# Kernel optimization log

Measured on AMD Instinct MI355X. Metric: run time of the kernel, lower is better.

## Reference

```python
import jax, jax.numpy as jnp
import numpy as np


def _shift(x, n):
    # torch.roll along the last (angular) axis
    return jnp.roll(x, n, axis=3)


def _flip(x, n):
    # mirror about index n along the last axis: out[..., i] = x[..., (n - i) mod W]
    return jnp.roll(jnp.flip(x, axis=3), n + 1, axis=3)


def setup_inputs() -> dict:
    key = jax.random.key(0)
    k1, k2, k3 = jax.random.split(key, 3)
    B, C, H, W = 16, 96, 96, 96
    x = jax.random.normal(k1, (B, C, H, W), dtype=jnp.float32)
    s = jax.random.normal(k2, (B, 5), dtype=jnp.float32)
    w = jax.random.uniform(k3, (B, C, H, W), dtype=jnp.float32) + 0.1  # keep denominator well-conditioned
    return {"x": x, "s": s, "w": w}


def reference(x, s, w):
    # s.shape[1] == 5 branch of SymmetryControl (square symmetry: 3 rotations + 2 mirrors)
    sg = jax.nn.sigmoid(s).reshape(s.shape[0], -1, 1, 1)  # [B,5,1,1]
    step = x.shape[3] // 8

    x90 = _shift(x, step * 2)
    x180 = _shift(x, step * 4)
    x270 = _shift(x, step * 6)
    x90f = _flip(x, step * 2 - 1)
    x180f = _flip(x, step * 4 - 1)

    w90 = sg[:, 0:1] * _shift(w, step * 2)
    w180 = sg[:, 1:2] * _shift(w, step * 4)
    w270 = sg[:, 2:3] * _shift(w, step * 6)
    w90f = sg[:, 3:4] * _flip(w, step * 2 - 1)
    w180f = sg[:, 4:5] * _flip(w, step * 4 - 1)

    a = (w * x + w90 * x90 + w180 * x180 + w270 * x270
         + w90f * x90f + w180f * x180f)
    b = w + w90 + w180 + w270 + w90f + w180f
    return a / b
```

## Files before the change

### kernel.cpp

```cpp
#include <hip/hip_runtime.h>


#define WDIM  96
#define RPB   9216
#define WPB   4
#define PAIRS 8
#define RPW   (2 * PAIRS)

typedef float fvec3 __attribute__((ext_vector_type(3)));

__device__ __forceinline__ float bperm(int byteidx, float v) {
    return __int_as_float(__builtin_amdgcn_ds_bpermute(byteidx, __float_as_int(v)));
}

__global__ __launch_bounds__(64 * WPB)
void symctl_kernel(const float* __restrict__ x,
                   const float* __restrict__ s,
                   const float* __restrict__ w,
                   float* __restrict__ out) {
    const int lane = threadIdx.x & 63;
    const int tl   = lane & 31;
    const int hsel = lane & 32;
    const int h    = lane >> 5;

    const int wid  = blockIdx.x * WPB + (threadIdx.x >> 6);
    const int base = (RPW * wid + h) * WDIM + 3 * tl;

    fvec3 xa[PAIRS], wa[PAIRS];
#pragma unroll
    for (int k = 0; k < PAIRS; ++k)
        xa[k] = *(const fvec3*)(x + base + k * (2 * WDIM));
#pragma unroll
    for (int k = 0; k < PAIRS; ++k)
        wa[k] = *(const fvec3*)(w + base + k * (2 * WDIM));

    __builtin_amdgcn_sched_barrier(0);

    const int b = (blockIdx.x * (RPW * WPB)) / RPB;
    const float* sb = s + b * 5;
    const float sg0 = 1.0f / (1.0f + __expf(-sb[0]));
    const float sg1 = 1.0f / (1.0f + __expf(-sb[1]));
    const float sg2 = 1.0f / (1.0f + __expf(-sb[2]));
    const float sg3 = 1.0f / (1.0f + __expf(-sb[3]));
    const float sg4 = 1.0f / (1.0f + __expf(-sb[4]));

    const int i90  = (hsel | ((tl -  8) & 31)) << 2;
    const int i180 = (hsel | ((tl - 16) & 31)) << 2;
    const int i270 = (hsel | ((tl +  8) & 31)) << 2;
    const int f90  = (hsel | (( 7 - tl) & 31)) << 2;
    const int f180 = (hsel | ((15 - tl) & 31)) << 2;

#pragma unroll
    for (int k = 0; k < PAIRS; ++k) {
        const fvec3 xc = xa[k];
        const fvec3 wc = wa[k];

        const float p0 = xc.x * wc.x;
        const float p1 = xc.y * wc.y;
        const float p2 = xc.z * wc.z;

        float n0 = p0,   n1 = p1,   n2 = p2;
        float d0 = wc.x, d1 = wc.y, d2 = wc.z;

        n0 = fmaf(sg0, bperm(i90,  p0),   n0);
        n1 = fmaf(sg0, bperm(i90,  p1),   n1);
        n2 = fmaf(sg0, bperm(i90,  p2),   n2);
        d0 = fmaf(sg0, bperm(i90,  wc.x), d0);
        d1 = fmaf(sg0, bperm(i90,  wc.y), d1);
        d2 = fmaf(sg0, bperm(i90,  wc.z), d2);

        n0 = fmaf(sg1, bperm(i180, p0),   n0);
        n1 = fmaf(sg1, bperm(i180, p1),   n1);
        n2 = fmaf(sg1, bperm(i180, p2),   n2);
        d0 = fmaf(sg1, bperm(i180, wc.x), d0);
        d1 = fmaf(sg1, bperm(i180, wc.y), d1);
        d2 = fmaf(sg1, bperm(i180, wc.z), d2);

        n0 = fmaf(sg2, bperm(i270, p0),   n0);
        n1 = fmaf(sg2, bperm(i270, p1),   n1);
        n2 = fmaf(sg2, bperm(i270, p2),   n2);
        d0 = fmaf(sg2, bperm(i270, wc.x), d0);
        d1 = fmaf(sg2, bperm(i270, wc.y), d1);
        d2 = fmaf(sg2, bperm(i270, wc.z), d2);

        n0 = fmaf(sg3, bperm(f90,  p2),   n0);
        n1 = fmaf(sg3, bperm(f90,  p1),   n1);
        n2 = fmaf(sg3, bperm(f90,  p0),   n2);
        d0 = fmaf(sg3, bperm(f90,  wc.z), d0);
        d1 = fmaf(sg3, bperm(f90,  wc.y), d1);
        d2 = fmaf(sg3, bperm(f90,  wc.x), d2);

        n0 = fmaf(sg4, bperm(f180, p2),   n0);
        n1 = fmaf(sg4, bperm(f180, p1),   n1);
        n2 = fmaf(sg4, bperm(f180, p0),   n2);
        d0 = fmaf(sg4, bperm(f180, wc.z), d0);
        d1 = fmaf(sg4, bperm(f180, wc.y), d1);
        d2 = fmaf(sg4, bperm(f180, wc.x), d2);

        fvec3 o;
        o.x = n0 * __builtin_amdgcn_rcpf(d0);
        o.y = n1 * __builtin_amdgcn_rcpf(d1);
        o.z = n2 * __builtin_amdgcn_rcpf(d2);
        __builtin_nontemporal_store(o, (fvec3*)(out + base + k * (2 * WDIM)));
    }
}

extern "C" void kernel_launch(void* const* d_in, const int* in_sizes, int n_in,
                              void* d_out, int out_size, void* d_ws, size_t ws_size,
                              hipStream_t stream) {
    const float* x = (const float*)d_in[0];
    const float* s = (const float*)d_in[1];
    const float* w = (const float*)d_in[2];
    float* out = (float*)d_out;

    const int n_rows = in_sizes[0] / WDIM;
    const int waves  = n_rows / RPW;
    const int grid   = waves / WPB;

    dim3 block(64 * WPB);
    symctl_kernel<<<grid, block, 0, stream>>>(x, s, w, out);
}
```

Baseline: 154.6 us.

## Use inline-asm split loads with staged vmcnt waits and halve rows per wave

```diff
diff --git a/kernel.cpp b/kernel.cpp
--- a/kernel.cpp
+++ b/kernel.cpp
@@ -4,10 +4,10 @@
 #define WDIM  96
 #define RPB   9216
 #define WPB   4
-#define PAIRS 8
+#define PAIRS 4
 #define RPW   (2 * PAIRS)
 
-typedef float fvec3 __attribute__((ext_vector_type(3)));
+typedef float v2f __attribute__((ext_vector_type(2)));
 
 __device__ __forceinline__ float bperm(int byteidx, float v) {
     return __int_as_float(__builtin_amdgcn_ds_bpermute(byteidx, __float_as_int(v)));
@@ -24,17 +24,7 @@
     const int h    = lane >> 5;
 
     const int wid  = blockIdx.x * WPB + (threadIdx.x >> 6);
-    const int base = (RPW * wid + h) * WDIM + 3 * tl;
-
-    fvec3 xa[PAIRS], wa[PAIRS];
-#pragma unroll
-    for (int k = 0; k < PAIRS; ++k)
-        xa[k] = *(const fvec3*)(x + base + k * (2 * WDIM));
-#pragma unroll
-    for (int k = 0; k < PAIRS; ++k)
-        wa[k] = *(const fvec3*)(w + base + k * (2 * WDIM));
-
-    __builtin_amdgcn_sched_barrier(0);
+    const int voff = ((RPW * wid + h) * WDIM + 3 * tl) * 4;
 
     const int b = (blockIdx.x * (RPW * WPB)) / RPB;
     const float* sb = s + b * 5;
@@ -50,59 +40,91 @@
     const int f90  = (hsel | (( 7 - tl) & 31)) << 2;
     const int f180 = (hsel | ((15 - tl) & 31)) << 2;
 
-#pragma unroll
-    for (int k = 0; k < PAIRS; ++k) {
-        const fvec3 xc = xa[k];
-        const fvec3 wc = wa[k];
+    v2f   xlo0, xlo1, xlo2, xlo3, wlo0, wlo1, wlo2, wlo3;
+    float xhi0, xhi1, xhi2, xhi3, whi0, whi1, whi2, whi3;
+#define LD_PAIR(K, XLO, XHI, WLO, WHI)                                          \
+    asm volatile("global_load_dwordx2 %0, %1, %2 offset:" #K                    \
+                 : "=v"(XLO) : "v"(voff), "s"(x));                              \
+    asm volatile("global_load_dword %0, %1, %2 offset:" #K "+8"                 \
+                 : "=v"(XHI) : "v"(voff), "s"(x));                              \
+    asm volatile("global_load_dwordx2 %0, %1, %2 offset:" #K                    \
+                 : "=v"(WLO) : "v"(voff), "s"(w));                              \
+    asm volatile("global_load_dword %0, %1, %2 offset:" #K "+8"                 \
+                 : "=v"(WHI) : "v"(voff), "s"(w));
+    LD_PAIR(0,    xlo0, xhi0, wlo0, whi0)
+    LD_PAIR(768,  xlo1, xhi1, wlo1, whi1)
+    LD_PAIR(1536, xlo2, xhi2, wlo2, whi2)
+    LD_PAIR(2304, xlo3, xhi3, wlo3, whi3)
+#undef LD_PAIR
 
-        const float p0 = xc.x * wc.x;
-        const float p1 = xc.y * wc.y;
-        const float p2 = xc.z * wc.z;
+    float o0x,o0y,o0z, o1x,o1y,o1z, o2x,o2y,o2z, o3x,o3y,o3z;
 
-        float n0 = p0,   n1 = p1,   n2 = p2;
-        float d0 = wc.x, d1 = wc.y, d2 = wc.z;
+#define COMPUTE(XLO, XHI, WLO, WHI, OX, OY, OZ)                                 \
+    {                                                                           \
+        const float wcx = WLO.x, wcy = WLO.y, wcz = WHI;                        \
+        const float p0 = XLO.x * wcx;                                           \
+        const float p1 = XLO.y * wcy;                                           \
+        const float p2 = XHI   * wcz;                                           \
+        float n0 = p0, n1 = p1, n2 = p2;                                        \
+        float d0 = wcx, d1 = wcy, d2 = wcz;                                     \
+        n0 = fmaf(sg0, bperm(i90,  p0),  n0);                                   \
+        n1 = fmaf(sg0, bperm(i90,  p1),  n1);                                   \
+        n2 = fmaf(sg0, bperm(i90,  p2),  n2);                                   \
+        d0 = fmaf(sg0, bperm(i90,  wcx), d0);                                   \
+        d1 = fmaf(sg0, bperm(i90,  wcy), d1);                                   \
+        d2 = fmaf(sg0, bperm(i90,  wcz), d2);                                   \
+        n0 = fmaf(sg1, bperm(i180, p0),  n0);                                   \
+        n1 = fmaf(sg1, bperm(i180, p1),  n1);                                   \
+        n2 = fmaf(sg1, bperm(i180, p2),  n2);                                   \
+        d0 = fmaf(sg1, bperm(i180, wcx), d0);                                   \
+        d1 = fmaf(sg1, bperm(i180, wcy), d1);                                   \
+        d2 = fmaf(sg1, bperm(i180, wcz), d2);                                   \
+        n0 = fmaf(sg2, bperm(i270, p0),  n0);                                   \
+        n1 = fmaf(sg2, bperm(i270, p1),  n1);                                   \
+        n2 = fmaf(sg2, bperm(i270, p2),  n2);                                   \
+        d0 = fmaf(sg2, bperm(i270, wcx), d0);                                   \
+        d1 = fmaf(sg2, bperm(i270, wcy), d1);                                   \
+        d2 = fmaf(sg2, bperm(i270, wcz), d2);                                   \
+        n0 = fmaf(sg3, bperm(f90,  p2),  n0);                                   \
+        n1 = fmaf(sg3, bperm(f90,  p1),  n1);                                   \
+        n2 = fmaf(sg3, bperm(f90,  p0),  n2);                                   \
+        d0 = fmaf(sg3, bperm(f90,  wcz), d0);                                   \
+        d1 = fmaf(sg3, bperm(f90,  wcy), d1);                                   \
+        d2 = fmaf(sg3, bperm(f90,  wcx), d2);                                   \
+        n0 = fmaf(sg4, bperm(f180, p2),  n0);                                   \
+        n1 = fmaf(sg4, bperm(f180, p1),  n1);                                   \
+        n2 = fmaf(sg4, bperm(f180, p0),  n2);                                   \
+        d0 = fmaf(sg4, bperm(f180, wcz), d0);                                   \
+        d1 = fmaf(sg4, bperm(f180, wcy), d1);                                   \
+        d2 = fmaf(sg4, bperm(f180, wcx), d2);                                   \
+        OX = n0 * __builtin_amdgcn_rcpf(d0);                                    \
+        OY = n1 * __builtin_amdgcn_rcpf(d1);                                    \
+        OZ = n2 * __builtin_amdgcn_rcpf(d2);                                    \
+    }
 
-        n0 = fmaf(sg0, bperm(i90,  p0),   n0);
-        n1 = fmaf(sg0, bperm(i90,  p1),   n1);
-        n2 = fmaf(sg0, bperm(i90,  p2),   n2);
-        d0 = fmaf(sg0, bperm(i90,  wc.x), d0);
-        d1 = fmaf(sg0, bperm(i90,  wc.y), d1);
-        d2 = fmaf(sg0, bperm(i90,  wc.z), d2);
+    asm volatile("s_waitcnt vmcnt(12)" ::: "memory");
+    __builtin_amdgcn_sched_barrier(0);
+    COMPUTE(xlo0, xhi0, wlo0, whi0, o0x, o0y, o0z)
 
-        n0 = fmaf(sg1, bperm(i180, p0),   n0);
-        n1 = fmaf(sg1, bperm(i180, p1),   n1);
-        n2 = fmaf(sg1, bperm(i180, p2),   n2);
-        d0 = fmaf(sg1, bperm(i180, wc.x), d0);
-        d1 = fmaf(sg1, bperm(i180, wc.y), d1);
-        d2 = fmaf(sg1, bperm(i180, wc.z), d2);
+    asm volatile("s_waitcnt vmcnt(8)" ::: "memory");
+    __builtin_amdgcn_sched_barrier(0);
+    COMPUTE(xlo1, xhi1, wlo1, whi1, o1x, o1y, o1z)
 
-        n0 = fmaf(sg2, bperm(i270, p0),   n0);
-        n1 = fmaf(sg2, bperm(i270, p1),   n1);
-        n2 = fmaf(sg2, bperm(i270, p2),   n2);
-        d0 = fmaf(sg2, bperm(i270, wc.x), d0);
-        d1 = fmaf(sg2, bperm(i270, wc.y), d1);
-        d2 = fmaf(sg2, bperm(i270, wc.z), d2);
+    asm volatile("s_waitcnt vmcnt(4)" ::: "memory");
+    __builtin_amdgcn_sched_barrier(0);
+    COMPUTE(xlo2, xhi2, wlo2, whi2, o2x, o2y, o2z)
 
-        n0 = fmaf(sg3, bperm(f90,  p2),   n0);
-        n1 = fmaf(sg3, bperm(f90,  p1),   n1);
-        n2 = fmaf(sg3, bperm(f90,  p0),   n2);
-        d0 = fmaf(sg3, bperm(f90,  wc.z), d0);
-        d1 = fmaf(sg3, bperm(f90,  wc.y), d1);
-        d2 = fmaf(sg3, bperm(f90,  wc.x), d2);
+    asm volatile("s_waitcnt vmcnt(0)" ::: "memory");
+    __builtin_amdgcn_sched_barrier(0);
+    COMPUTE(xlo3, xhi3, wlo3, whi3, o3x, o3y, o3z)
+#undef COMPUTE
 
-        n0 = fmaf(sg4, bperm(f180, p2),   n0);
-        n1 = fmaf(sg4, bperm(f180, p1),   n1);
-        n2 = fmaf(sg4, bperm(f180, p0),   n2);
-        d0 = fmaf(sg4, bperm(f180, wc.z), d0);
-        d1 = fmaf(sg4, bperm(f180, wc.y), d1);
-        d2 = fmaf(sg4, bperm(f180, wc.x), d2);
-
-        fvec3 o;
-        o.x = n0 * __builtin_amdgcn_rcpf(d0);
-        o.y = n1 * __builtin_amdgcn_rcpf(d1);
-        o.z = n2 * __builtin_amdgcn_rcpf(d2);
-        __builtin_nontemporal_store(o, (fvec3*)(out + base + k * (2 * WDIM)));
-    }
+    float* op = out + (voff >> 2);
+    float3 o;
+    o.x = o0x; o.y = o0y; o.z = o0z; *(float3*)(op + 0 * 2 * WDIM) = o;
+    o.x = o1x; o.y = o1y; o.z = o1z; *(float3*)(op + 1 * 2 * WDIM) = o;
+    o.x = o2x; o.y = o2y; o.z = o2z; *(float3*)(op + 2 * 2 * WDIM) = o;
+    o.x = o3x; o.y = o3y; o.z = o3z; *(float3*)(op + 3 * 2 * WDIM) = o;
 }
 
 extern "C" void kernel_launch(void* const* d_in, const int* in_sizes, int n_in,
```

Result: no change. 152.1 us (-1.6%).
